# Performance work log

Measured on AMD Instinct MI355X. Metric: run time of the kernel, lower is better.

## Reference

```python
import jax, jax.numpy as jnp
import numpy as np

B, C, H, W = 4, 64, 256, 256
P, PRIOR, HID, HEADS, NPROMPT = 4, 64, 128, 4, 4
TOKEN = C * P * P  # 1024
RATIO = 0.25


def _patchify(x):
    b, c, h, w = x.shape
    gh, gw = h // P, w // P
    t = x.reshape(b, c, gh, P, gw, P).transpose(0, 2, 4, 1, 3, 5).reshape(b, gh * gw, c * P * P)
    return t, (b, c, gh, gw)


def _unpatchify(t, meta):
    b, c, gh, gw = meta
    return t.reshape(b, gh, gw, c, P, P).transpose(0, 3, 1, 4, 2, 5).reshape(b, c, gh * P, gw * P)


def _coords(gh, gw):
    ys = (jnp.arange(gh, dtype=jnp.float32) + 0.5) / gh
    xs = (jnp.arange(gw, dtype=jnp.float32) + 0.5) / gw
    yy, xx = jnp.meshgrid(ys, xs, indexing='ij')
    return jnp.stack([yy.ravel(), xx.ravel()], axis=-1)  # [N, 2]


def setup_inputs():
    key = jax.random.key(0)
    ks = iter(jax.random.split(key, 32))
    rn = lambda *s: jax.random.normal(next(ks), s, jnp.float32)
    w = lambda *s: rn(*s) * 0.02
    z = lambda *s: jnp.zeros(s, jnp.float32)
    return dict(
        vis_feat=rn(B, C, H, W),
        ir_feat=rn(B, C, H, W),
        prompt_bank=w(NPROMPT, PRIOR),
        Wr=w(2 * C, NPROMPT), br=z(NPROMPT),
        br_Wtok=w(2, 2 * TOKEN, HID), br_Wpri=w(2, PRIOR, HID), br_Wco=w(2, 2, HID),
        br_bs=z(2, HID), br_Wout=w(2, HID), br_bout=z(2),
        br_Wq=w(2, TOKEN, HID), br_Wk=w(2, TOKEN, HID), br_Wv=w(2, TOKEN, HID),
        br_Wo=w(2, HID, TOKEN), br_Wint=w(2, PRIOR, HID),
        br_Wbyp=w(2, 2 * TOKEN, TOKEN), br_bbyp=z(2, TOKEN),
        conv1_w=w(C, C, 3, 3), conv1_b=z(C),
        conv2_w=w(C, C, 3, 3), conv2_b=z(C),
        Wa1=w(PRIOR, 2 * C), ba1=z(2 * C),
        Wa2=w(2 * C, 2 * C), ba2=z(2 * C),
    )


def reference(vis_feat, ir_feat, prompt_bank, Wr, br, br_Wtok, br_Wpri, br_Wco, br_bs, br_Wout, br_bout, br_Wq, br_Wk, br_Wv, br_Wo, br_Wint, br_Wbyp, br_bbyp, conv1_w, conv1_b, conv2_w, conv2_b, Wa1, ba1, Wa2, ba2):
    # intent router: pooled features -> prompt mixture -> intent vector
    pooled = jnp.concatenate([vis_feat.mean((2, 3)), ir_feat.mean((2, 3))], -1)  # [B, 2C]
    prompt_weight = jax.nn.softmax(pooled @ Wr + br, -1)  # [B, NPROMPT]
    intent = prompt_weight @ prompt_bank  # [B, PRIOR]

    def split(x):
        F = jnp.fft.fft2(x)
        return jnp.abs(F), jnp.angle(F)

    vamp, vph = split(vis_feat)
    iamp, iph = split(ir_feat)

    def fuse(vm, im, i):
        vt, meta = _patchify(vm)
        it_, _ = _patchify(im)
        b, c, gh, gw = meta
        n = gh * gw
        coords = _coords(gh, gw)
        # token score net: tokens + intent + coord embedding -> scalar score per token
        h = (jnp.concatenate([vt, it_], -1) @ br_Wtok[i]
             + (intent @ br_Wpri[i])[:, None, :]
             + (coords @ br_Wco[i])[None] + br_bs[i])
        score = jax.nn.gelu(h) @ br_Wout[i] + br_bout[i]  # [B, N]
        k = max(1, int(n * RATIO))
        topk_val, topk_idx = jax.lax.top_k(score, k)
        gth = lambda t: jnp.take_along_axis(t, topk_idx[:, :, None], axis=1)
        vs, irs = gth(vt), gth(it_)  # [B, k, TOKEN]
        # selected-token cross attention (vis queries, ir keys/values), intent-modulated
        dh = HID // HEADS
        hd = lambda x, Wm: (x @ Wm).reshape(b, k, HEADS, dh)
        q, kk, vv = hd(vs, br_Wq[i]), hd(irs, br_Wk[i]), hd(irs, br_Wv[i])
        attn = jax.nn.softmax(jnp.einsum('bqhd,bkhd->bhqk', q, kk) / jnp.float32(np.sqrt(dh)), -1)
        o = jnp.einsum('bhqk,bkhd->bqhd', attn, vv).reshape(b, k, HID)
        o = o + (intent @ br_Wint[i])[:, None, :]
        fused_sel = vs + o @ br_Wo[i]  # [B, k, TOKEN]
        # lightweight bypass on all tokens (gated blend), then scatter selected back
        g = jax.nn.sigmoid(jnp.concatenate([vt, it_], -1) @ br_Wbyp[i] + br_bbyp[i])
        full = g * vt + (1.0 - g) * it_
        full = full.at[jnp.arange(b)[:, None], topk_idx].set(fused_sel)
        return _unpatchify(full, meta)

    famp = fuse(vamp, iamp, 0)
    fph = fuse(vph, iph, 1)
    fph = jnp.arctan2(jnp.sin(fph), jnp.cos(fph))  # phase wrap to (-pi, pi]
    spec = jax.lax.complex(famp * jnp.cos(fph), famp * jnp.sin(fph))
    spatial = jnp.fft.ifft2(spec).real

    conv = lambda x, wgt, bia: jax.lax.conv_general_dilated(
        x, wgt, (1, 1), 'SAME', dimension_numbers=('NCHW', 'OIHW', 'NCHW')) + bia[None, :, None, None]
    y = conv(jax.nn.relu(conv(spatial, conv1_w, conv1_b)), conv2_w, conv2_b)
    aff = jax.nn.gelu(intent @ Wa1 + ba1) @ Wa2 + ba2  # [B, 2C]
    gamma, beta = aff[:, :C], aff[:, C:]
    y = y * (1.0 + 0.1 * jnp.tanh(gamma))[:, :, None, None] + 0.1 * beta[:, :, None, None]
    return y + 0.5 * (vis_feat + ir_feat)
```

## Files before the change

kernel.cpp:

```cpp
#include <hip/hip_runtime.h>

typedef unsigned int uint;
typedef unsigned long long u64;
typedef __attribute__((ext_vector_type(8))) short short8;
typedef __attribute__((ext_vector_type(4))) float f32x4;

__device__ __forceinline__ uint brev8(uint x){ return __brev(x) >> 24; }
__device__ __forceinline__ float geluf(float x){
  return 0.5f*x*(1.f + tanhf(0.7978845608028654f*(x + 0.044715f*x*x*x)));
}
__device__ __forceinline__ unsigned short f2bf(float f){
  unsigned u = __float_as_uint(f);
  unsigned r = u + 0x7FFFu + ((u >> 16) & 1u);
  return (unsigned short)(r >> 16);
}
__device__ __forceinline__ float bf2f(unsigned short u){
  return __uint_as_float((uint)u << 16);
}

__global__ __launch_bounds__(256) void kern_pool(const float* __restrict__ vis,
                                                 const float* __restrict__ irf,
                                                 float* __restrict__ pooled){
  __shared__ float red[256];
  int bc = blockIdx.x;
  int b = bc >> 7, cc = bc & 127;
  const float* src = (cc < 64) ? (vis + (size_t)(b*64+cc)*65536)
                               : (irf + (size_t)(b*64+(cc-64))*65536);
  float s = 0.f;
  for (int i = threadIdx.x; i < 65536; i += 256) s += src[i];
  red[threadIdx.x] = s;
  __syncthreads();
  for (int off = 128; off > 0; off >>= 1){
    if (threadIdx.x < off) red[threadIdx.x] += red[threadIdx.x + off];
    __syncthreads();
  }
  if (threadIdx.x == 0) pooled[bc] = red[0] * (1.f/65536.f);
}

__global__ __launch_bounds__(256) void kern_small(const float* __restrict__ pooled,
    const float* __restrict__ Wr, const float* __restrict__ br,
    const float* __restrict__ bank, const float* __restrict__ Wpri,
    const float* __restrict__ Wint, const float* __restrict__ Wa1,
    const float* __restrict__ ba1, const float* __restrict__ Wa2,
    const float* __restrict__ ba2,
    float* __restrict__ IP, float* __restrict__ IPint,
    float* __restrict__ modg, float* __restrict__ modb){
  __shared__ float logit_s[16];
  __shared__ float pw_s[16];
  __shared__ float intent_s[4][64];
  __shared__ float t1_s[4][128];
  int t = threadIdx.x;
  if (t < 16){
    int b = t >> 2, j = t & 3;
    float s = br[j];
    for (int k = 0; k < 128; ++k) s += pooled[b*128+k]*Wr[k*4+j];
    logit_s[t] = s;
  }
  __syncthreads();
  if (t < 4){
    int b = t;
    float m = logit_s[b*4];
    for (int j = 1; j < 4; ++j) m = fmaxf(m, logit_s[b*4+j]);
    float e[4], sum = 0.f;
    for (int j = 0; j < 4; ++j){ e[j] = expf(logit_s[b*4+j]-m); sum += e[j]; }
    for (int j = 0; j < 4; ++j) pw_s[b*4+j] = e[j]/sum;
  }
  __syncthreads();
  {
    int b = t >> 6, p = t & 63;
    float s = 0.f;
    for (int j = 0; j < 4; ++j) s += pw_s[b*4+j]*bank[j*64+p];
    intent_s[b][p] = s;
  }
  __syncthreads();
  for (int o = t; o < 1024; o += 256){
    int i = o >> 9, rem = o & 511, b = rem >> 7, n = rem & 127;
    float s1 = 0.f, s2 = 0.f;
    for (int p = 0; p < 64; ++p){
      float iv = intent_s[b][p];
      s1 += iv * Wpri[(i*64+p)*128 + n];
      s2 += iv * Wint[(i*64+p)*128 + n];
    }
    IP[o] = s1; IPint[o] = s2;
  }
  for (int o = t; o < 512; o += 256){
    int b = o >> 7, n = o & 127;
    float s = ba1[n];
    for (int p = 0; p < 64; ++p) s += intent_s[b][p]*Wa1[p*128+n];
    t1_s[b][n] = geluf(s);
  }
  __syncthreads();
  for (int o = t; o < 512; o += 256){
    int b = o >> 7, n = o & 127;
    float s = ba2[n];
    for (int p = 0; p < 128; ++p) s += t1_s[b][p]*Wa2[p*128+n];
    if (n < 64) modg[b*64+n] = 1.f + 0.1f*tanhf(s);
    else        modb[b*64+(n-64)] = 0.1f*s;
  }
}

__global__ __launch_bounds__(256) void kern_fft_rows_fwd(const float* __restrict__ x,
    float* __restrict__ sre, float* __restrict__ sim){
  __shared__ float re[2][256], im[2][256];
  __shared__ float twr[128], twi[128];
  int t = threadIdx.x;
  if (t < 128){
    float a = -6.2831853071795864f * (float)t * (1.f/256.f);
    sincosf(a, &twi[t], &twr[t]);
  }
  int r = t >> 7, jj = t & 127;
  size_t row = (size_t)blockIdx.x*2 + r;
  {
    const float* xp = x + row*256;
    re[r][jj] = xp[jj]; re[r][jj+128] = xp[jj+128];
    im[r][jj] = 0.f;    im[r][jj+128] = 0.f;
  }
  __syncthreads();
  for (int s = 0; s < 8; ++s){
    int half = 128 >> s;
    int j = jj & (half-1);
    int g = jj >> (7-s);
    int k = (g << (8-s)) + j;
    int m = j << s;
    float wc = twr[m], ws = twi[m];
    float are = re[r][k],      aim = im[r][k];
    float bre = re[r][k+half], bim = im[r][k+half];
    re[r][k] = are + bre; im[r][k] = aim + bim;
    float tr = are - bre, ti = aim - bim;
    re[r][k+half] = tr*wc - ti*ws;
    im[r][k+half] = tr*ws + ti*wc;
    __syncthreads();
  }
  {
    float* orp = sre + row*256; float* oip = sim + row*256;
    int w1 = jj, w2 = jj + 128;
    orp[w1] = re[r][brev8(w1)]; oip[w1] = im[r][brev8(w1)];
    orp[w2] = re[r][brev8(w2)]; oip[w2] = im[r][brev8(w2)];
  }
}

__global__ __launch_bounds__(256) void kern_ifft_rows_spec(const float* __restrict__ famp,
    const float* __restrict__ fph, float* __restrict__ sre, float* __restrict__ sim){
  __shared__ float re[4][256], im[4][256];
  __shared__ float twr[128], twi[128];
  int t = threadIdx.x;
  if (t < 128){
    float a = -6.2831853071795864f * (float)t * (1.f/256.f);
    sincosf(a, &twi[t], &twr[t]);
  }
  int R = blockIdx.x * 4;
  {
    int r = t >> 6, q = t & 63;
    int row = R + r;
    int bc = row >> 8, h = row & 255;
    int b = bc >> 6, c = bc & 63;
    size_t addr = ((size_t)(b*4096 + (h>>2)*64 + q))*1024 + c*16 + (h&3)*4;
    float4 a4 = *(const float4*)(famp + addr);
    float4 p4 = *(const float4*)(fph + addr);
    float sn, cs;
    sincosf(p4.x, &sn, &cs); re[r][4*q+0] = a4.x*cs; im[r][4*q+0] = a4.x*sn;
    sincosf(p4.y, &sn, &cs); re[r][4*q+1] = a4.y*cs; im[r][4*q+1] = a4.y*sn;
    sincosf(p4.z, &sn, &cs); re[r][4*q+2] = a4.z*cs; im[r][4*q+2] = a4.z*sn;
    sincosf(p4.w, &sn, &cs); re[r][4*q+3] = a4.w*cs; im[r][4*q+3] = a4.w*sn;
  }
  __syncthreads();
  for (int s = 0; s < 8; ++s){
    int half = 128 >> s;
    #pragma unroll
    for (int bi0 = 0; bi0 < 2; ++bi0){
      int bi = t + bi0*256;
      int r = bi >> 7, tj = bi & 127;
      int j = tj & (half-1);
      int g = tj >> (7-s);
      int k = (g << (8-s)) + j;
      int m = j << s;
      float wc = twr[m], ws = -twi[m];
      float are = re[r][k],      aim = im[r][k];
      float bre = re[r][k+half], bim = im[r][k+half];
      re[r][k] = are + bre; im[r][k] = aim + bim;
      float tr = are - bre, ti = aim - bim;
      re[r][k+half] = tr*wc - ti*ws;
      im[r][k+half] = tr*ws + ti*wc;
    }
    __syncthreads();
  }
  {
    int r = t >> 6, q = t & 63;
    size_t row = (size_t)R + r;
    float4 vr, vi;
    vr.x = re[r][brev8(4*q+0)]; vi.x = im[r][brev8(4*q+0)];
    vr.y = re[r][brev8(4*q+1)]; vi.y = im[r][brev8(4*q+1)];
    vr.z = re[r][brev8(4*q+2)]; vi.z = im[r][brev8(4*q+2)];
    vr.w = re[r][brev8(4*q+3)]; vi.w = im[r][brev8(4*q+3)];
    *(float4*)(sre + row*256 + 4*q) = vr;
    *(float4*)(sim + row*256 + 4*q) = vi;
  }
}

template<int DIR>
__global__ __launch_bounds__(256) void kern_fft_cols(const float* __restrict__ sre,
    const float* __restrict__ sim, void* __restrict__ out0, void* __restrict__ out1){
  __shared__ float reL[256*17];
  __shared__ float imL[256*17];
  __shared__ float twr[128], twi[128];
  int t = threadIdx.x;
  if (t < 128){
    float a = -6.2831853071795864f * (float)t * (1.f/256.f);
    sincosf(a, &twi[t], &twr[t]);
  }
  int img = blockIdx.x >> 4;
  int c0 = (blockIdx.x & 15) * 16;
  {
    const float* pr = sre + ((size_t)img*256 + t)*256 + c0;
    const float* pi = sim + ((size_t)img*256 + t)*256 + c0;
    #pragma unroll
    for (int p = 0; p < 4; ++p){
      float4 vr = *(const float4*)(pr + 4*p);
      float4 vi = *(const float4*)(pi + 4*p);
      int base = t*17 + 4*p;
      reL[base+0]=vr.x; reL[base+1]=vr.y; reL[base+2]=vr.z; reL[base+3]=vr.w;
      imL[base+0]=vi.x; imL[base+1]=vi.y; imL[base+2]=vi.z; imL[base+3]=vi.w;
    }
  }
  __syncthreads();
  int col = t & 15, tb = t >> 4;
  for (int s = 0; s < 8; ++s){
    int half = 128 >> s;
    #pragma unroll
    for (int it = 0; it < 8; ++it){
      int tj = tb + it*16;
      int j = tj & (half-1);
      int g = tj >> (7-s);
      int k = (g << (8-s)) + j;
      int m = j << s;
      float wc = twr[m];
      float ws = (DIR == 0) ? twi[m] : -twi[m];
      int i0 = k*17 + col, i1 = (k+half)*17 + col;
      float are = reL[i0], aim = imL[i0];
      float bre = reL[i1], bim = imL[i1];
      reL[i0] = are + bre; imL[i0] = aim + bim;
      float tr = are - bre, ti = aim - bim;
      reL[i1] = tr*wc - ti*ws;
      imL[i1] = tr*ws + ti*wc;
    }
    __syncthreads();
  }
  int b = img >> 6, c = img & 63;
  int h = t; int src = (int)brev8((uint)h);
  if (DIR == 0){
    unsigned short* oa = (unsigned short*)out0;
    unsigned short* op = (unsigned short*)out1;
    int gy = h >> 2, py = h & 3;
    #pragma unroll
    for (int p = 0; p < 4; ++p){
      int base = src*17 + 4*p;
      float a0, a1, a2, a3, p0, p1, p2, p3;
      float rr, ii;
      rr = reL[base+0]; ii = imL[base+0]; a0 = sqrtf(rr*rr+ii*ii); p0 = atan2f(ii, rr);
      rr = reL[base+1]; ii = imL[base+1]; a1 = sqrtf(rr*rr+ii*ii); p1 = atan2f(ii, rr);
      rr = reL[base+2]; ii = imL[base+2]; a2 = sqrtf(rr*rr+ii*ii); p2 = atan2f(ii, rr);
      rr = reL[base+3]; ii = imL[base+3]; a3 = sqrtf(rr*rr+ii*ii); p3 = atan2f(ii, rr);
      size_t addr = ((size_t)(b*4096 + gy*64 + (c0>>2) + p))*1024 + c*16 + py*4;
      uint2 av, pv;
      av.x = (uint)f2bf(a0) | ((uint)f2bf(a1) << 16);
      av.y = (uint)f2bf(a2) | ((uint)f2bf(a3) << 16);
      pv.x = (uint)f2bf(p0) | ((uint)f2bf(p1) << 16);
      pv.y = (uint)f2bf(p2) | ((uint)f2bf(p3) << 16);
      *(uint2*)(oa + addr) = av;
      *(uint2*)(op + addr) = pv;
    }
  } else {
    float* op = (float*)out0 + ((size_t)img*256 + h)*256 + c0;
    #pragma unroll
    for (int p = 0; p < 4; ++p){
      int base = src*17 + 4*p;
      float4 v;
      v.x = reL[base+0]*(1.f/65536.f);
      v.y = reL[base+1]*(1.f/65536.f);
      v.z = reL[base+2]*(1.f/65536.f);
      v.w = reL[base+3]*(1.f/65536.f);
      *(float4*)(op + 4*p) = v;
    }
  }
}

struct TRS {
  const float* src[10];
  unsigned short* dst[10];
  int K[10], N[10];
  int start[11];
};
__global__ __launch_bounds__(256) void kern_tr(TRS p){
  __shared__ float lds[32][33];
  int bid = blockIdx.x;
  int e = 0;
  while (bid >= p.start[e+1]) ++e;
  int tloc = bid - p.start[e];
  int tilesN = p.N[e] >> 5;
  int tn = tloc % tilesN, tk = tloc / tilesN;
  int k0 = tk << 5, n0 = tn << 5;
  const float* src = p.src[e];
  unsigned short* dst = p.dst[e];
  int K = p.K[e], N = p.N[e];
  int r = threadIdx.x >> 5, c = threadIdx.x & 31;
  #pragma unroll
  for (int i = 0; i < 4; ++i)
    lds[r + 8*i][c] = src[(size_t)(k0 + r + 8*i)*N + n0 + c];
  __syncthreads();
  #pragma unroll
  for (int i = 0; i < 4; ++i)
    dst[(size_t)(n0 + r + 8*i)*K + k0 + c] = f2bf(lds[c][r + 8*i]);
}

struct GP2 {
  const unsigned short* A0[6];
  const unsigned short* A1[2];
  const unsigned short* Bt[6];
  float* Cm[6];
  const int* idxp[6];
  const float* ep0[2];
  const float* ep1[2];
  const float* ep2[2];
  int N, K;
};

template<int AMODE, int EPI>
__global__ __launch_bounds__(256) void kern_mgemm2(GP2 p){
  __shared__ __align__(16) unsigned short Asb[64*64];
  __shared__ __align__(16) unsigned short Bsb[128*64];
  __shared__ int idx_s[64];
  int z = blockIdx.z;
  const unsigned short* A0 = p.A0[z];
  const unsigned short* Bt = p.Bt[z];
  float* Cm = p.Cm[z];
  int tid = threadIdx.x;
  int m0 = blockIdx.x * 64;
  int n0 = blockIdx.y * 128;
  int lane = tid & 63, w = tid >> 6;
  int wr = w & 1, wc = w >> 1;
  int lr = lane & 15, ql = lane >> 4;

  if (AMODE == 2){
    if (tid < 64){
      int m = m0 + tid;
      idx_s[tid] = p.idxp[z][(m >> 10)*1024 + (m & 1023)];
    }
    __syncthreads();
  }
  int gb = m0 >> 10;

  f32x4 acc[2][4];
  #pragma unroll
  for (int i = 0; i < 2; ++i)
    #pragma unroll
    for (int j = 0; j < 4; ++j) acc[i][j] = (f32x4){0.f,0.f,0.f,0.f};

  int kh = tid & 7;
  int rA = tid >> 3;
  for (int k0 = 0; k0 < p.K; k0 += 64){
    #pragma unroll
    for (int s = 0; s < 2; ++s){
      int m = rA + 32*s;
      const unsigned short* ap;
      if (AMODE == 1){
        const unsigned short* srcp = (k0 < 1024) ? A0 : p.A1[z];
        ap = srcp + (size_t)(m0+m)*1024 + (k0 & 1023) + kh*8;
      } else {
        ap = A0 + ((size_t)(gb << 12) + idx_s[m])*(size_t)p.K + k0 + kh*8;
      }
      short8 v = *(const short8*)ap;
      int byte = m*128 + ((kh*16) ^ ((m & 7)*16));
      *(short8*)((char*)Asb + byte) = v;
    }
    #pragma unroll
    for (int s = 0; s < 4; ++s){
      int n = rA + 32*s;
      short8 v = *(const short8*)(Bt + (size_t)(n0+n)*p.K + k0 + kh*8);
      int byte = n*128 + ((kh*16) ^ ((n & 7)*16));
      *(short8*)((char*)Bsb + byte) = v;
    }
    __syncthreads();
    short8 af[2][2], bf[4][2];
    #pragma unroll
    for (int fm = 0; fm < 2; ++fm){
      int row = wr*32 + fm*16 + lr;
      #pragma unroll
      for (int kq = 0; kq < 2; ++kq){
        int byte = row*128 + ((kq*64 + ql*16) ^ ((row & 7)*16));
        af[fm][kq] = *(const short8*)((const char*)Asb + byte);
      }
    }
    #pragma unroll
    for (int fn = 0; fn < 4; ++fn){
      int row = wc*64 + fn*16 + lr;
      #pragma unroll
      for (int kq = 0; kq < 2; ++kq){
        int byte = row*128 + ((kq*64 + ql*16) ^ ((row & 7)*16));
        bf[fn][kq] = *(const short8*)((const char*)Bsb + byte);
      }
    }
    #pragma unroll
    for (int kq = 0; kq < 2; ++kq)
      #pragma unroll
      for (int fm = 0; fm < 2; ++fm)
        #pragma unroll
        for (int fn = 0; fn < 4; ++fn)
          acc[fm][fn] = __builtin_amdgcn_mfma_f32_16x16x32_bf16(af[fm][kq], bf[fn][kq],
                                                                acc[fm][fn], 0, 0, 0);
    __syncthreads();
  }

  #pragma unroll
  for (int fm = 0; fm < 2; ++fm){
    #pragma unroll
    for (int fn = 0; fn < 4; ++fn){
      int n = n0 + wc*64 + fn*16 + lr;
      #pragma unroll
      for (int reg = 0; reg < 4; ++reg){
        int m = m0 + wr*32 + fm*16 + ql*4 + reg;
        float v = acc[fm][fn][reg];
        if (EPI == 0){
          Cm[(size_t)m*p.N + n] = v;
        } else {
          int bl = m >> 12, g = m & 4095;
          int gy = g >> 6, gx = g & 63;
          float cy = ((float)gy + 0.5f)*(1.f/64.f);
          float cx = ((float)gx + 0.5f)*(1.f/64.f);
          float o = v + p.ep0[z][bl*128 + n] + cy*p.ep1[z][n]
                  + cx*p.ep1[z][128 + n] + p.ep2[z][n];
          Cm[(size_t)m*128 + n] = o;
        }
      }
    }
  }
}

struct GP3 {
  const unsigned short* A0[2];
  const unsigned short* A1[2];
  const unsigned short* Bt[2];
  float* Cm[2];
  const float* bias[2];
  const unsigned short* vt[2];
  const unsigned short* it[2];
  int K;
};

__global__ __launch_bounds__(256) void kern_mgemm3(GP3 p){
  __shared__ __align__(16) unsigned short Asb[128*64];
  __shared__ __align__(16) unsigned short Bsb[128*64];
  int z = blockIdx.z;
  const unsigned short* Bt = p.Bt[z];
  float* Cm = p.Cm[z];
  int tid = threadIdx.x;
  int m0 = blockIdx.x * 128;
  int n0 = blockIdx.y * 128;
  int lane = tid & 63, w = tid >> 6;
  int wr = w & 1, wc = w >> 1;
  int lr = lane & 15, ql = lane >> 4;

  f32x4 acc[4][4];
  #pragma unroll
  for (int i = 0; i < 4; ++i)
    #pragma unroll
    for (int j = 0; j < 4; ++j) acc[i][j] = (f32x4){0.f,0.f,0.f,0.f};

  int kh = tid & 7;
  int rA = tid >> 3;
  for (int k0 = 0; k0 < p.K; k0 += 64){
    const unsigned short* Asrc = (k0 < 1024) ? p.A0[z] : p.A1[z];
    int kk = (k0 & 1023) + kh*8;
    #pragma unroll
    for (int s = 0; s < 4; ++s){
      int m = rA + 32*s;
      short8 v = *(const short8*)(Asrc + (size_t)(m0+m)*1024 + kk);
      int byte = m*128 + ((kh*16) ^ ((m & 7)*16));
      *(short8*)((char*)Asb + byte) = v;
    }
    #pragma unroll
    for (int s = 0; s < 4; ++s){
      int n = rA + 32*s;
      short8 v = *(const short8*)(Bt + (size_t)(n0+n)*p.K + k0 + kh*8);
      int byte = n*128 + ((kh*16) ^ ((n & 7)*16));
      *(short8*)((char*)Bsb + byte) = v;
    }
    __syncthreads();
    short8 af[4][2], bf[4][2];
    #pragma unroll
    for (int fm = 0; fm < 4; ++fm){
      int row = wr*64 + fm*16 + lr;
      #pragma unroll
      for (int kq = 0; kq < 2; ++kq){
        int byte = row*128 + ((kq*64 + ql*16) ^ ((row & 7)*16));
        af[fm][kq] = *(const short8*)((const char*)Asb + byte);
      }
    }
    #pragma unroll
    for (int fn = 0; fn < 4; ++fn){
      int row = wc*64 + fn*16 + lr;
      #pragma unroll
      for (int kq = 0; kq < 2; ++kq){
        int byte = row*128 + ((kq*64 + ql*16) ^ ((row & 7)*16));
        bf[fn][kq] = *(const short8*)((const char*)Bsb + byte);
      }
    }
    #pragma unroll
    for (int kq = 0; kq < 2; ++kq)
      #pragma unroll
      for (int fm = 0; fm < 4; ++fm)
        #pragma unroll
        for (int fn = 0; fn < 4; ++fn)
          acc[fm][fn] = __builtin_amdgcn_mfma_f32_16x16x32_bf16(af[fm][kq], bf[fn][kq],
                                                                acc[fm][fn], 0, 0, 0);
    __syncthreads();
  }

  const unsigned short* vtp = p.vt[z];
  const unsigned short* itp = p.it[z];
  #pragma unroll
  for (int fm = 0; fm < 4; ++fm){
    #pragma unroll
    for (int fn = 0; fn < 4; ++fn){
      int n = n0 + wc*64 + fn*16 + lr;
      float bia = p.bias[z][n];
      #pragma unroll
      for (int reg = 0; reg < 4; ++reg){
        int m = m0 + wr*64 + fm*16 + ql*4 + reg;
        size_t off = (size_t)m*1024 + n;
        float vt = bf2f(vtp[off]);
        float it = bf2f(itp[off]);
        float gg = 1.f/(1.f + expf(-(acc[fm][fn][reg] + bia)));
        Cm[off] = gg*vt + (1.f-gg)*it;
      }
    }
  }
}

struct SCP {
  const float* A0[2];
  const float* Bm[2];
  float* Cm[2];
  const int* idxp[2];
  const unsigned short* vtb[2];
};

__global__ __launch_bounds__(256) void kern_scat(SCP p){
  __shared__ __align__(16) unsigned short Asb[64*40];
  __shared__ __align__(16) unsigned short Bsb[128*40];
  __shared__ int idx_s[64];
  int z = blockIdx.z;
  const float* A0 = p.A0[z];
  const float* Bm = p.Bm[z];
  float* Cm = p.Cm[z];
  int tid = threadIdx.x;
  int m0 = blockIdx.y * 64;
  int n0 = blockIdx.x * 128;
  int lane = tid & 63, w = tid >> 6;
  int wr = w & 1, wc = w >> 1;
  int lr = lane & 15, ql = lane >> 4;
  if (tid < 64){
    int m = m0 + tid;
    idx_s[tid] = p.idxp[z][(m >> 10)*1024 + (m & 1023)];
  }
  __syncthreads();
  int gb = m0 >> 10;

  f32x4 acc[2][4];
  #pragma unroll
  for (int i = 0; i < 2; ++i)
    #pragma unroll
    for (int j = 0; j < 4; ++j) acc[i][j] = (f32x4){0.f,0.f,0.f,0.f};

  for (int k0 = 0; k0 < 128; k0 += 32){
    {
      int m = tid & 63;
      int khh = (tid >> 6) * 8;
      const float* ap = A0 + (size_t)(m0+m)*128 + k0 + khh;
      float4 f0 = *(const float4*)ap;
      float4 f1 = *(const float4*)(ap + 4);
      short8 v;
      v[0]=(short)f2bf(f0.x); v[1]=(short)f2bf(f0.y);
      v[2]=(short)f2bf(f0.z); v[3]=(short)f2bf(f0.w);
      v[4]=(short)f2bf(f1.x); v[5]=(short)f2bf(f1.y);
      v[6]=(short)f2bf(f1.z); v[7]=(short)f2bf(f1.w);
      *(short8*)&Asb[m*40 + khh] = v;
    }
    #pragma unroll
    for (int e0 = 0; e0 < 512; e0 += 256){
      int e = e0 + tid;
      int n = e & 127;
      int khh = (e >> 7) * 8;
      const float* bp = Bm + (size_t)(k0+khh)*1024 + n0 + n;
      short8 v;
      #pragma unroll
      for (int j = 0; j < 8; ++j) v[j] = (short)f2bf(bp[(size_t)j*1024]);
      *(short8*)&Bsb[n*40 + khh] = v;
    }
    __syncthreads();
    short8 af[2], bf[4];
    #pragma unroll
    for (int fr = 0; fr < 2; ++fr)
      af[fr] = *(const short8*)&Asb[(wr*32 + fr*16 + lr)*40 + ql*8];
    #pragma unroll
    for (int fc = 0; fc < 4; ++fc)
      bf[fc] = *(const short8*)&Bsb[(wc*64 + fc*16 + lr)*40 + ql*8];
    #pragma unroll
    for (int fr = 0; fr < 2; ++fr)
      #pragma unroll
      for (int fc = 0; fc < 4; ++fc)
        acc[fr][fc] = __builtin_amdgcn_mfma_f32_16x16x32_bf16(af[fr], bf[fc],
                                                              acc[fr][fc], 0, 0, 0);
    __syncthreads();
  }

  #pragma unroll
  for (int fr = 0; fr < 2; ++fr){
    #pragma unroll
    for (int fc = 0; fc < 4; ++fc){
      int n = n0 + wc*64 + fc*16 + lr;
      #pragma unroll
      for (int reg = 0; reg < 4; ++reg){
        int mloc = wr*32 + fr*16 + ql*4 + reg;
        int gt = idx_s[mloc];
        size_t off = ((size_t)(gb << 12) + gt)*1024 + n;
        Cm[off] = acc[fr][fc][reg] + bf2f(p.vtb[z][off]);
      }
    }
  }
}

__global__ __launch_bounds__(64) void kern_score(const float* __restrict__ h,
    const float* __restrict__ wout, const float* __restrict__ bout,
    float* __restrict__ score, int Mper){
  int m = blockIdx.x, br = blockIdx.y, t = threadIdx.x;
  const float* hp = h + ((size_t)br*Mper + m)*128;
  const float* wp = wout + br*128;
  float s = geluf(hp[t])*wp[t] + geluf(hp[t+64])*wp[t+64];
  #pragma unroll
  for (int off = 32; off > 0; off >>= 1) s += __shfl_down(s, off);
  if (t == 0) score[(size_t)br*Mper + m] = s + bout[br];
}

__global__ __launch_bounds__(1024) void kern_topk(const float* __restrict__ score,
    int* __restrict__ idx_out){
  __shared__ u64 keys[4096];
  int b = blockIdx.x, t = threadIdx.x;
  for (int i = t; i < 4096; i += 1024){
    float s = score[b*4096 + i];
    uint u = __float_as_uint(s);
    uint msk = (u & 0x80000000u) ? ~u : (u | 0x80000000u);
    keys[i] = ((u64)msk << 32) | (uint)(4095 - i);
  }
  __syncthreads();
  for (int k = 2; k <= 4096; k <<= 1){
    for (int j = k >> 1; j > 0; j >>= 1){
      for (int i = t; i < 4096; i += 1024){
        int l = i ^ j;
        if (l > i){
          u64 a = keys[i], c = keys[l];
          bool descB = ((i & k) == 0);
          bool sw = descB ? (a < c) : (a > c);
          if (sw){ keys[i] = c; keys[l] = a; }
        }
      }
      __syncthreads();
    }
  }
  idx_out[b*1024 + t] = 4095 - (int)(keys[t] & 0xFFFFFFFFu);
}

__global__ __launch_bounds__(128) void kern_attn_part(const float* __restrict__ qb,
    const float* __restrict__ kb, const float* __restrict__ vb,
    float* __restrict__ paoa, float* __restrict__ pml){
  __shared__ float Ks[64][32];
  __shared__ float Vs[64][32];
  int t = threadIdx.x;
  int hh = blockIdx.y;
  int zc = blockIdx.z;
  int zf = zc >> 2, c = zc & 3;
  size_t boff = (size_t)zf*131072;
  int jq = blockIdx.x*128 + t;
  float qv[32];
  {
    const float4* qp = (const float4*)(qb + boff + (size_t)jq*128 + hh*32);
    #pragma unroll
    for (int d = 0; d < 8; ++d) ((float4*)qv)[d] = qp[d];
  }
  float mrun = -3.0e38f, lrun = 0.f;
  float oa[32];
  #pragma unroll
  for (int d = 0; d < 32; ++d) oa[d] = 0.f;
  for (int kt = 0; kt < 4; ++kt){
    int k0 = c*256 + kt*64;
    #pragma unroll
    for (int rep = 0; rep < 4; ++rep){
      int f = t + rep*128;
      int r = f >> 3, q4 = f & 7;
      size_t base = boff + (size_t)(k0 + r)*128 + hh*32 + 4*q4;
      *(float4*)&Ks[r][4*q4] = *(const float4*)(kb + base);
      *(float4*)&Vs[r][4*q4] = *(const float4*)(vb + base);
    }
    __syncthreads();
    #pragma unroll
    for (int st = 0; st < 4; ++st){
      float s[16];
      #pragma unroll
      for (int j = 0; j < 16; ++j){
        float v = 0.f;
        #pragma unroll
        for (int d = 0; d < 32; ++d) v += qv[d]*Ks[st*16+j][d];
        s[j] = v * 0.17677669529663687f;
      }
      float mt = s[0];
      #pragma unroll
      for (int j = 1; j < 16; ++j) mt = fmaxf(mt, s[j]);
      float mnew = fmaxf(mrun, mt);
      float alpha = expf(mrun - mnew);
      lrun *= alpha;
      #pragma unroll
      for (int d = 0; d < 32; ++d) oa[d] *= alpha;
      #pragma unroll
      for (int j = 0; j < 16; ++j){
        float pe = expf(s[j] - mnew);
        lrun += pe;
        #pragma unroll
        for (int d = 0; d < 32; ++d) oa[d] += pe*Vs[st*16+j][d];
      }
      mrun = mnew;
    }
    __syncthreads();
  }
  size_t rec = (((size_t)zf*4 + hh)*4 + c)*1024 + jq;
  float* pp = paoa + rec*32;
  #pragma unroll
  for (int d = 0; d < 8; ++d) ((float4*)pp)[d] = ((float4*)oa)[d];
  pml[rec*2]   = mrun;
  pml[rec*2+1] = lrun;
}

__global__ __launch_bounds__(256) void kern_attn_comb(const float* __restrict__ paoa,
    const float* __restrict__ pml, float* __restrict__ ob,
    const float* __restrict__ ipint, int PB, int b0){
  int t = threadIdx.x;
  int hh = blockIdx.y, zf = blockIdx.z;
  int jq = blockIdx.x*256 + t;
  size_t rbase = (((size_t)zf*4 + hh)*4)*1024 + jq;
  float mc[4], lc[4];
  #pragma unroll
  for (int c = 0; c < 4; ++c){
    mc[c] = pml[(rbase + c*1024)*2];
    lc[c] = pml[(rbase + c*1024)*2 + 1];
  }
  float M = fmaxf(fmaxf(mc[0], mc[1]), fmaxf(mc[2], mc[3]));
  float wgt[4], L = 0.f;
  #pragma unroll
  for (int c = 0; c < 4; ++c){ wgt[c] = expf(mc[c] - M); L += lc[c]*wgt[c]; }
  float inv = 1.f/L;
  int br = (zf >= PB) ? 1 : 0;
  int bb = zf - br*PB;
  const float* ip = ipint + br*512 + (b0+bb)*128 + hh*32;
  float* op = ob + (size_t)zf*131072 + (size_t)jq*128 + hh*32;
  #pragma unroll
  for (int d = 0; d < 32; ++d){
    float o = 0.f;
    #pragma unroll
    for (int c = 0; c < 4; ++c) o += paoa[(rbase + c*1024)*32 + d]*wgt[c];
    op[d] = o*inv + ip[d];
  }
}

__global__ __launch_bounds__(256) void kern_wt(const float* __restrict__ w1,
    const float* __restrict__ w2, unsigned short* __restrict__ wt){
  int blk = blockIdx.x;
  const float* src = (blk < 9) ? w1 : w2;
  int tap = blk - (blk < 9 ? 0 : 9);
  unsigned short* dst = wt + (blk < 9 ? 0 : 36864) + tap*4096;
  for (int e = threadIdx.x; e < 4096; e += 256){
    dst[e] = f2bf(src[(size_t)e*9 + tap]);
  }
}

template<int MODE>
__global__ __launch_bounds__(256) void kern_cmfma(const float* __restrict__ in,
    const unsigned short* __restrict__ wt, const float* __restrict__ bias,
    float* __restrict__ out,
    const float* __restrict__ modg, const float* __restrict__ modb,
    const float* __restrict__ vis, const float* __restrict__ irf){
  __shared__ __align__(16) unsigned short ins[64][268];
  int t = threadIdx.x;
  int y = blockIdx.x, b = blockIdx.y;
  int lane = t & 63, w = t >> 6;
  int wc = w & 1, wx = w >> 1;
  int lr = lane & 15, ql = lane >> 4;

  f32x4 acc[2][8];
  #pragma unroll
  for (int f = 0; f < 2; ++f)
    #pragma unroll
    for (int xf = 0; xf < 8; ++xf) acc[f][xf] = (f32x4){0.f,0.f,0.f,0.f};

  for (int dy = 0; dy < 3; ++dy){
    int yy = y + dy - 1;
    if (yy < 0 || yy > 255) continue;
    const float* src = in + ((size_t)(b*64)*256 + yy)*256;
    #pragma unroll
    for (int s = 0; s < 16; ++s){
      int e = t + s*256;
      int ci = e >> 6, q = e & 63;
      float4 f4 = *(const float4*)(src + (size_t)ci*65536 + 4*q);
      uint lo = (uint)f2bf(f4.x) | ((uint)f2bf(f4.y) << 16);
      uint hi = (uint)f2bf(f4.z) | ((uint)f2bf(f4.w) << 16);
      *(uint2*)&ins[ci][4*q + 4] = make_uint2(lo, hi);
    }
    if (t < 128){
      int r = t & 63;
      ins[r][(t >> 6) ? 260 : 3] = 0;
    }
    __syncthreads();
    short8 wf[2][3][2];
    #pragma unroll
    for (int kk = 0; kk < 2; ++kk)
      #pragma unroll
      for (int dx = 0; dx < 3; ++dx)
        #pragma unroll
        for (int f = 0; f < 2; ++f)
          wf[kk][dx][f] = *(const short8*)(wt +
            (size_t)((dy*3 + dx)*64 + 32*wc + 16*f + lr)*64 + kk*32 + ql*8);
    #pragma unroll
    for (int kk = 0; kk < 2; ++kk){
      const unsigned short* bp = &ins[kk*32 + ql*8][0];
      #pragma unroll
      for (int dx = 0; dx < 3; ++dx){
        int xb = 128*wx + lr + dx + 3;
        #pragma unroll
        for (int xf = 0; xf < 8; ++xf){
          int xi = xb + 16*xf;
          short8 bf;
          #pragma unroll
          for (int e = 0; e < 8; ++e) bf[e] = (short)bp[e*268 + xi];
          acc[0][xf] = __builtin_amdgcn_mfma_f32_16x16x32_bf16(wf[kk][dx][0], bf,
                                                               acc[0][xf], 0, 0, 0);
          acc[1][xf] = __builtin_amdgcn_mfma_f32_16x16x32_bf16(wf[kk][dx][1], bf,
                                                               acc[1][xf], 0, 0, 0);
        }
      }
    }
    __syncthreads();
  }

  #pragma unroll
  for (int f = 0; f < 2; ++f){
    #pragma unroll
    for (int xf = 0; xf < 8; ++xf){
      int x = 128*wx + 16*xf + lr;
      #pragma unroll
      for (int reg = 0; reg < 4; ++reg){
        int co = 32*wc + 16*f + ql*4 + reg;
        float v = acc[f][xf][reg] + bias[co];
        size_t oi = ((size_t)(b*64 + co)*256 + y)*256 + x;
        if (MODE == 1){
          out[oi] = fmaxf(v, 0.f);
        } else {
          out[oi] = v*modg[b*64+co] + modb[b*64+co] + 0.5f*(vis[oi] + irf[oi]);
        }
      }
    }
  }
}

extern "C" void kernel_launch(void* const* d_in, const int* in_sizes, int n_in,
                              void* d_out, int out_size, void* d_ws, size_t ws_size,
                              hipStream_t stream){
  (void)in_sizes; (void)n_in; (void)out_size;
  const float* vis  = (const float*)d_in[0];
  const float* irf  = (const float*)d_in[1];
  const float* bank = (const float*)d_in[2];
  const float* Wr   = (const float*)d_in[3];
  const float* br   = (const float*)d_in[4];
  const float* Wtok = (const float*)d_in[5];
  const float* Wpri = (const float*)d_in[6];
  const float* Wco  = (const float*)d_in[7];
  const float* bs   = (const float*)d_in[8];
  const float* Wout = (const float*)d_in[9];
  const float* bout = (const float*)d_in[10];
  const float* Wq   = (const float*)d_in[11];
  const float* Wk   = (const float*)d_in[12];
  const float* Wv   = (const float*)d_in[13];
  const float* Wo   = (const float*)d_in[14];
  const float* Wint = (const float*)d_in[15];
  const float* Wbyp = (const float*)d_in[16];
  const float* bbyp = (const float*)d_in[17];
  const float* c1w  = (const float*)d_in[18];
  const float* c1b  = (const float*)d_in[19];
  const float* c2w  = (const float*)d_in[20];
  const float* c2b  = (const float*)d_in[21];
  const float* Wa1  = (const float*)d_in[22];
  const float* ba1  = (const float*)d_in[23];
  const float* Wa2  = (const float*)d_in[24];
  const float* ba2  = (const float*)d_in[25];

  auto needB = [](int PB)->size_t{
    return ((size_t)PB*14755840 + 2792448) * 4;
  };
  const int PB = (ws_size >= needB(4)) ? 4 : (ws_size >= needB(2)) ? 2 : 1;

  float* ws = (float*)d_ws;
  const size_t PLF = (size_t)PB*4194304;
  float* PH4 = ws;
  unsigned short* ABV = (unsigned short*)(ws + PLF);
  unsigned short* PBV = ABV + PLF;
  unsigned short* ABI = PBV + PLF;
  unsigned short* PBI = ABI + PLF;
  float* S0 = ws + PLF;
  float* S1 = S0 + PLF;
  float* sm = ws + 3*PLF;
  float* hbuf  = sm; sm += (size_t)2*PB*524288;
  float* qbuf  = sm; sm += (size_t)2*PB*131072;
  float* kbuf  = sm; sm += (size_t)2*PB*131072;
  float* vbuf  = sm; sm += (size_t)2*PB*131072;
  float* obuf  = sm; sm += (size_t)2*PB*131072;
  float* score = sm; sm += (size_t)2*PB*4096;
  int*   idxb  = (int*)sm; sm += (size_t)2*PB*1024;
  float* pml   = sm; sm += (size_t)PB*65536;
  unsigned short* BTtok = (unsigned short*)sm;
  unsigned short* BTbyp = BTtok + 524288;
  unsigned short* BTq   = BTbyp + 4194304;
  unsigned short* BTk   = BTq + 262144;
  unsigned short* BTv   = BTk + 262144;
  sm += 2752512;
  float* pooled= sm; sm += 512;
  float* IP    = sm; sm += 1024;
  float* IPint = sm; sm += 1024;
  float* modg  = sm; sm += 256;
  float* modb  = sm; sm += 256;
  unsigned short* wtb = (unsigned short*)sm; sm += 36864;
  float* paoa = hbuf;

  kern_pool <<<512, 256, 0, stream>>>(vis, irf, pooled);
  kern_small<<<1, 256, 0, stream>>>(pooled, Wr, br, bank, Wpri, Wint,
                                    Wa1, ba1, Wa2, ba2, IP, IPint, modg, modb);
  kern_wt   <<<18, 256, 0, stream>>>(c1w, c2w, wtb);
  {
    TRS tr{};
    const float* srcs[10] = {Wtok, Wtok+262144, Wbyp, Wbyp+2097152,
                             Wq, Wq+131072, Wk, Wk+131072, Wv, Wv+131072};
    unsigned short* dsts[10] = {BTtok, BTtok+262144, BTbyp, BTbyp+2097152,
                                BTq, BTq+131072, BTk, BTk+131072, BTv, BTv+131072};
    int Ks[10] = {2048,2048,2048,2048,1024,1024,1024,1024,1024,1024};
    int Ns[10] = {128,128,1024,1024,128,128,128,128,128,128};
    int tiles[10] = {256,256,2048,2048,128,128,128,128,128,128};
    int acc0 = 0;
    for (int i = 0; i < 10; ++i){
      tr.src[i] = srcs[i]; tr.dst[i] = dsts[i];
      tr.K[i] = Ks[i]; tr.N[i] = Ns[i];
      tr.start[i] = acc0; acc0 += tiles[i];
    }
    tr.start[10] = acc0;
    kern_tr<<<acc0, 256, 0, stream>>>(tr);
  }

  for (int b0 = 0; b0 < 4; b0 += PB){
    const float* vis_b = vis + (size_t)b0*4194304;
    const float* ir_b  = irf + (size_t)b0*4194304;
    float* OUT = (float*)d_out + (size_t)b0*4194304;

    kern_fft_rows_fwd<<<PB*8192, 256, 0, stream>>>(vis_b, OUT, PH4);
    kern_fft_cols<0> <<<PB*1024, 256, 0, stream>>>(OUT, PH4, ABV, PBV);
    kern_fft_rows_fwd<<<PB*8192, 256, 0, stream>>>(ir_b, OUT, PH4);
    kern_fft_cols<0> <<<PB*1024, 256, 0, stream>>>(OUT, PH4, ABI, PBI);

    {
      GP2 p{};
      p.A0[0]=ABV; p.A1[0]=ABI; p.A0[1]=PBV; p.A1[1]=PBI;
      for (int z = 0; z < 2; ++z){
        p.Bt[z] = BTtok + (size_t)z*262144;
        p.Cm[z] = hbuf + (size_t)z*PB*524288;
        p.ep0[z] = IP + z*512 + b0*128;
        p.ep1[z] = Wco + z*256;
        p.ep2[z] = bs + z*128;
      }
      p.N = 128; p.K = 2048;
      kern_mgemm2<1,1><<<dim3(PB*64, 1, 2), 256, 0, stream>>>(p);
    }
    kern_score<<<dim3(PB*4096, 2), 64, 0, stream>>>(hbuf, Wout, bout, score, PB*4096);
    kern_topk <<<2*PB, 1024, 0, stream>>>(score, idxb);
    {
      GP3 p{};
      p.A0[0]=ABV; p.A1[0]=ABI; p.A0[1]=PBV; p.A1[1]=PBI;
      p.vt[0]=ABV; p.it[0]=ABI; p.vt[1]=PBV; p.it[1]=PBI;
      p.Cm[0]=OUT; p.Cm[1]=PH4;
      for (int z = 0; z < 2; ++z){
        p.Bt[z] = BTbyp + (size_t)z*2097152;
        p.bias[z] = bbyp + z*1024;
      }
      p.K = 2048;
      kern_mgemm3<<<dim3(PB*32, 8, 2), 256, 0, stream>>>(p);
    }
    {
      GP2 p{};
      const unsigned short* Aplanes[6] = {ABV, ABI, ABI, PBV, PBI, PBI};
      const unsigned short* Bmats[6] = {BTq, BTk, BTv,
                                        BTq+131072, BTk+131072, BTv+131072};
      float* Cms[6] = {qbuf, kbuf, vbuf,
                       qbuf+(size_t)PB*131072, kbuf+(size_t)PB*131072,
                       vbuf+(size_t)PB*131072};
      for (int z = 0; z < 6; ++z){
        p.A0[z] = Aplanes[z]; p.Bt[z] = Bmats[z]; p.Cm[z] = Cms[z];
        p.idxp[z] = idxb + (z < 3 ? 0 : PB*1024);
      }
      p.N = 128; p.K = 1024;
      kern_mgemm2<2,0><<<dim3(PB*16, 1, 6), 256, 0, stream>>>(p);
    }
    kern_attn_part<<<dim3(8, 4, 2*PB*4), 128, 0, stream>>>(qbuf, kbuf, vbuf,
                                                           paoa, pml);
    kern_attn_comb<<<dim3(4, 4, 2*PB), 256, 0, stream>>>(paoa, pml, obuf,
                                                         IPint, PB, b0);
    {
      SCP p{};
      p.A0[0]=obuf; p.A0[1]=obuf+(size_t)PB*131072;
      p.Bm[0]=Wo; p.Bm[1]=Wo+131072;
      p.Cm[0]=OUT; p.Cm[1]=PH4;
      p.vtb[0]=ABV; p.vtb[1]=PBV;
      p.idxp[0]=idxb; p.idxp[1]=idxb+PB*1024;
      kern_scat<<<dim3(8, PB*16, 2), 256, 0, stream>>>(p);
    }

    kern_ifft_rows_spec<<<PB*4096, 256, 0, stream>>>(OUT, PH4, S0, S1);
    kern_fft_cols<1>   <<<PB*1024, 256, 0, stream>>>(S0, S1, OUT, nullptr);
  }

  kern_cmfma<1><<<dim3(256, 4), 256, 0, stream>>>((float*)d_out, wtb, c1b, ws,
                                                  nullptr, nullptr, nullptr, nullptr);
  kern_cmfma<2><<<dim3(256, 4), 256, 0, stream>>>(ws, wtb + 36864, c2b, (float*)d_out,
                                                  modg, modb, vis, irf);
}
```

Baseline: 1.419 ms.

## Fuse token-score GEMM into bypass GEMM by concatenating weight matrices

The score-hidden GEMM (Wtok, N=128) and the bypass gate GEMM (Wbyp, N=1024) share the same A operand, the concatenated vis/ir amplitude or phase tokens. They are merged into one launch by storing both transposed weights contiguously (N=1152) and adding a ninth column-block whose epilogue writes the hidden activations with the coordinate and intent bias terms. This avoids a separate kernel launch and lets both GEMMs run in one grid. The merged kernel now runs before top-k, which is valid because the bypass output does not depend on top-k, though the extra epilogue branch may add some register pressure.

```diff
diff --git a/kernel.cpp b/kernel.cpp
--- a/kernel.cpp
+++ b/kernel.cpp
@@ -1,6 +1,7 @@
 #include <hip/hip_runtime.h>
 
 typedef unsigned int uint;
+typedef unsigned short ushort;
 typedef unsigned long long u64;
 typedef __attribute__((ext_vector_type(8))) short short8;
 typedef __attribute__((ext_vector_type(4))) float f32x4;
@@ -9,12 +10,12 @@
 __device__ __forceinline__ float geluf(float x){
   return 0.5f*x*(1.f + tanhf(0.7978845608028654f*(x + 0.044715f*x*x*x)));
 }
-__device__ __forceinline__ unsigned short f2bf(float f){
+__device__ __forceinline__ ushort f2bf(float f){
   unsigned u = __float_as_uint(f);
   unsigned r = u + 0x7FFFu + ((u >> 16) & 1u);
-  return (unsigned short)(r >> 16);
-}
-__device__ __forceinline__ float bf2f(unsigned short u){
+  return (ushort)(r >> 16);
+}
+__device__ __forceinline__ float bf2f(ushort u){
   return __uint_as_float((uint)u << 16);
 }
 
@@ -248,8 +249,8 @@
   int b = img >> 6, c = img & 63;
   int h = t; int src = (int)brev8((uint)h);
   if (DIR == 0){
-    unsigned short* oa = (unsigned short*)out0;
-    unsigned short* op = (unsigned short*)out1;
+    ushort* oa = (ushort*)out0;
+    ushort* op = (ushort*)out1;
     int gy = h >> 2, py = h & 3;
     #pragma unroll
     for (int p = 0; p < 4; ++p){
@@ -286,7 +287,7 @@
 
 struct TRS {
   const float* src[10];
-  unsigned short* dst[10];
+  ushort* dst[10];
   int K[10], N[10];
   int start[11];
 };
@@ -300,7 +301,7 @@
   int tn = tloc % tilesN, tk = tloc / tilesN;
   int k0 = tk << 5, n0 = tn << 5;
   const float* src = p.src[e];
-  unsigned short* dst = p.dst[e];
+  ushort* dst = p.dst[e];
   int K = p.K[e], N = p.N[e];
   int r = threadIdx.x >> 5, c = threadIdx.x & 31;
   #pragma unroll
@@ -313,25 +314,20 @@
 }
 
 struct GP2 {
-  const unsigned short* A0[6];
-  const unsigned short* A1[2];
-  const unsigned short* Bt[6];
+  const ushort* A0[6];
+  const ushort* Bt[6];
   float* Cm[6];
   const int* idxp[6];
-  const float* ep0[2];
-  const float* ep1[2];
-  const float* ep2[2];
   int N, K;
 };
 
-template<int AMODE, int EPI>
 __global__ __launch_bounds__(256) void kern_mgemm2(GP2 p){
-  __shared__ __align__(16) unsigned short Asb[64*64];
-  __shared__ __align__(16) unsigned short Bsb[128*64];
+  __shared__ __align__(16) ushort Asb[64*64];
+  __shared__ __align__(16) ushort Bsb[128*64];
   __shared__ int idx_s[64];
   int z = blockIdx.z;
-  const unsigned short* A0 = p.A0[z];
-  const unsigned short* Bt = p.Bt[z];
+  const ushort* A0 = p.A0[z];
+  const ushort* Bt = p.Bt[z];
   float* Cm = p.Cm[z];
   int tid = threadIdx.x;
   int m0 = blockIdx.x * 64;
@@ -340,13 +336,11 @@
   int wr = w & 1, wc = w >> 1;
   int lr = lane & 15, ql = lane >> 4;
 
-  if (AMODE == 2){
-    if (tid < 64){
-      int m = m0 + tid;
-      idx_s[tid] = p.idxp[z][(m >> 10)*1024 + (m & 1023)];
-    }
-    __syncthreads();
-  }
+  if (tid < 64){
+    int m = m0 + tid;
+    idx_s[tid] = p.idxp[z][(m >> 10)*1024 + (m & 1023)];
+  }
+  __syncthreads();
   int gb = m0 >> 10;
 
   f32x4 acc[2][4];
@@ -361,13 +355,7 @@
     #pragma unroll
     for (int s = 0; s < 2; ++s){
       int m = rA + 32*s;
-      const unsigned short* ap;
-      if (AMODE == 1){
-        const unsigned short* srcp = (k0 < 1024) ? A0 : p.A1[z];
-        ap = srcp + (size_t)(m0+m)*1024 + (k0 & 1023) + kh*8;
-      } else {
-        ap = A0 + ((size_t)(gb << 12) + idx_s[m])*(size_t)p.K + k0 + kh*8;
-      }
+      const ushort* ap = A0 + ((size_t)(gb << 12) + idx_s[m])*(size_t)p.K + k0 + kh*8;
       short8 v = *(const short8*)ap;
       int byte = m*128 + ((kh*16) ^ ((m & 7)*16));
       *(short8*)((char*)Asb + byte) = v;
@@ -418,40 +406,32 @@
       #pragma unroll
       for (int reg = 0; reg < 4; ++reg){
         int m = m0 + wr*32 + fm*16 + ql*4 + reg;
-        float v = acc[fm][fn][reg];
-        if (EPI == 0){
-          Cm[(size_t)m*p.N + n] = v;
-        } else {
-          int bl = m >> 12, g = m & 4095;
-          int gy = g >> 6, gx = g & 63;
-          float cy = ((float)gy + 0.5f)*(1.f/64.f);
-          float cx = ((float)gx + 0.5f)*(1.f/64.f);
-          float o = v + p.ep0[z][bl*128 + n] + cy*p.ep1[z][n]
-                  + cx*p.ep1[z][128 + n] + p.ep2[z][n];
-          Cm[(size_t)m*128 + n] = o;
-        }
+        Cm[(size_t)m*p.N + n] = acc[fm][fn][reg];
       }
     }
   }
 }
 
 struct GP3 {
-  const unsigned short* A0[2];
-  const unsigned short* A1[2];
-  const unsigned short* Bt[2];
+  const ushort* A0[2];
+  const ushort* A1[2];
+  const ushort* Bt[2];
+  float* Ch[2];
   float* Cm[2];
+  const float* ep0[2];
+  const float* ep1[2];
+  const float* ep2[2];
   const float* bias[2];
-  const unsigned short* vt[2];
-  const unsigned short* it[2];
+  const ushort* vt[2];
+  const ushort* it[2];
   int K;
 };
 
 __global__ __launch_bounds__(256) void kern_mgemm3(GP3 p){
-  __shared__ __align__(16) unsigned short Asb[128*64];
-  __shared__ __align__(16) unsigned short Bsb[128*64];
+  __shared__ __align__(16) ushort Asb[128*64];
+  __shared__ __align__(16) ushort Bsb[128*64];
   int z = blockIdx.z;
-  const unsigned short* Bt = p.Bt[z];
-  float* Cm = p.Cm[z];
+  const ushort* Bt = p.Bt[z];
   int tid = threadIdx.x;
   int m0 = blockIdx.x * 128;
   int n0 = blockIdx.y * 128;
@@ -468,7 +448,7 @@
   int kh = tid & 7;
   int rA = tid >> 3;
   for (int k0 = 0; k0 < p.K; k0 += 64){
-    const unsigned short* Asrc = (k0 < 1024) ? p.A0[z] : p.A1[z];
+    const ushort* Asrc = (k0 < 1024) ? p.A0[z] : p.A1[z];
     int kk = (k0 & 1023) + kh*8;
     #pragma unroll
     for (int s = 0; s < 4; ++s){
@@ -515,22 +495,46 @@
     __syncthreads();
   }
 
-  const unsigned short* vtp = p.vt[z];
-  const unsigned short* itp = p.it[z];
-  #pragma unroll
-  for (int fm = 0; fm < 4; ++fm){
-    #pragma unroll
-    for (int fn = 0; fn < 4; ++fn){
-      int n = n0 + wc*64 + fn*16 + lr;
-      float bia = p.bias[z][n];
-      #pragma unroll
-      for (int reg = 0; reg < 4; ++reg){
-        int m = m0 + wr*64 + fm*16 + ql*4 + reg;
-        size_t off = (size_t)m*1024 + n;
-        float vt = bf2f(vtp[off]);
-        float it = bf2f(itp[off]);
-        float gg = 1.f/(1.f + expf(-(acc[fm][fn][reg] + bia)));
-        Cm[off] = gg*vt + (1.f-gg)*it;
+  if (blockIdx.y == 0){
+    float* Ch = p.Ch[z];
+    #pragma unroll
+    for (int fm = 0; fm < 4; ++fm){
+      #pragma unroll
+      for (int fn = 0; fn < 4; ++fn){
+        int n = wc*64 + fn*16 + lr;
+        #pragma unroll
+        for (int reg = 0; reg < 4; ++reg){
+          int m = m0 + wr*64 + fm*16 + ql*4 + reg;
+          int bl = m >> 12, g = m & 4095;
+          int gy = g >> 6, gx = g & 63;
+          float cy = ((float)gy + 0.5f)*(1.f/64.f);
+          float cx = ((float)gx + 0.5f)*(1.f/64.f);
+          float o = acc[fm][fn][reg] + p.ep0[z][bl*128 + n] + cy*p.ep1[z][n]
+                  + cx*p.ep1[z][128 + n] + p.ep2[z][n];
+          Ch[(size_t)m*128 + n] = o;
+        }
+      }
+    }
+  } else {
+    float* Cm = p.Cm[z];
+    const ushort* vtp = p.vt[z];
+    const ushort* itp = p.it[z];
+    int nb = n0 - 128;
+    #pragma unroll
+    for (int fm = 0; fm < 4; ++fm){
+      #pragma unroll
+      for (int fn = 0; fn < 4; ++fn){
+        int n = nb + wc*64 + fn*16 + lr;
+        float bia = p.bias[z][n];
+        #pragma unroll
+        for (int reg = 0; reg < 4; ++reg){
+          int m = m0 + wr*64 + fm*16 + ql*4 + reg;
+          size_t off = (size_t)m*1024 + n;
+          float vt = bf2f(vtp[off]);
+          float it = bf2f(itp[off]);
+          float gg = 1.f/(1.f + expf(-(acc[fm][fn][reg] + bia)));
+          Cm[off] = gg*vt + (1.f-gg)*it;
+        }
       }
     }
   }
@@ -541,12 +545,12 @@
   const float* Bm[2];
   float* Cm[2];
   const int* idxp[2];
-  const unsigned short* vtb[2];
+  const ushort* vtb[2];
 };
 
 __global__ __launch_bounds__(256) void kern_scat(SCP p){
-  __shared__ __align__(16) unsigned short Asb[64*40];
-  __shared__ __align__(16) unsigned short Bsb[128*40];
+  __shared__ __align__(16) ushort Asb[64*40];
+  __shared__ __align__(16) ushort Bsb[128*40];
   __shared__ int idx_s[64];
   int z = blockIdx.z;
   const float* A0 = p.A0[z];
@@ -770,11 +774,11 @@
 }
 
 __global__ __launch_bounds__(256) void kern_wt(const float* __restrict__ w1,
-    const float* __restrict__ w2, unsigned short* __restrict__ wt){
+    const float* __restrict__ w2, ushort* __restrict__ wt){
   int blk = blockIdx.x;
   const float* src = (blk < 9) ? w1 : w2;
   int tap = blk - (blk < 9 ? 0 : 9);
-  unsigned short* dst = wt + (blk < 9 ? 0 : 36864) + tap*4096;
+  ushort* dst = wt + (blk < 9 ? 0 : 36864) + tap*4096;
   for (int e = threadIdx.x; e < 4096; e += 256){
     dst[e] = f2bf(src[(size_t)e*9 + tap]);
   }
@@ -782,11 +786,11 @@
 
 template<int MODE>
 __global__ __launch_bounds__(256) void kern_cmfma(const float* __restrict__ in,
-    const unsigned short* __restrict__ wt, const float* __restrict__ bias,
+    const ushort* __restrict__ wt, const float* __restrict__ bias,
     float* __restrict__ out,
     const float* __restrict__ modg, const float* __restrict__ modb,
     const float* __restrict__ vis, const float* __restrict__ irf){
-  __shared__ __align__(16) unsigned short ins[64][268];
+  __shared__ __align__(16) ushort ins[64][268];
   int t = threadIdx.x;
   int y = blockIdx.x, b = blockIdx.y;
   int lane = t & 63, w = t >> 6;
@@ -828,7 +832,7 @@
             (size_t)((dy*3 + dx)*64 + 32*wc + 16*f + lr)*64 + kk*32 + ql*8);
     #pragma unroll
     for (int kk = 0; kk < 2; ++kk){
-      const unsigned short* bp = &ins[kk*32 + ql*8][0];
+      const ushort* bp = &ins[kk*32 + ql*8][0];
       #pragma unroll
       for (int dx = 0; dx < 3; ++dx){
         int xb = 128*wx + lr + dx + 3;
@@ -907,10 +911,10 @@
   float* ws = (float*)d_ws;
   const size_t PLF = (size_t)PB*4194304;
   float* PH4 = ws;
-  unsigned short* ABV = (unsigned short*)(ws + PLF);
-  unsigned short* PBV = ABV + PLF;
-  unsigned short* ABI = PBV + PLF;
-  unsigned short* PBI = ABI + PLF;
+  ushort* ABV = (ushort*)(ws + PLF);
+  ushort* PBV = ABV + PLF;
+  ushort* ABI = PBV + PLF;
+  ushort* PBI = ABI + PLF;
   float* S0 = ws + PLF;
   float* S1 = S0 + PLF;
   float* sm = ws + 3*PLF;
@@ -922,18 +926,17 @@
   float* score = sm; sm += (size_t)2*PB*4096;
   int*   idxb  = (int*)sm; sm += (size_t)2*PB*1024;
   float* pml   = sm; sm += (size_t)PB*65536;
-  unsigned short* BTtok = (unsigned short*)sm;
-  unsigned short* BTbyp = BTtok + 524288;
-  unsigned short* BTq   = BTbyp + 4194304;
-  unsigned short* BTk   = BTq + 262144;
-  unsigned short* BTv   = BTk + 262144;
+  ushort* BTcomb = (ushort*)sm;
+  ushort* BTq    = BTcomb + 4718592;
+  ushort* BTk    = BTq + 262144;
+  ushort* BTv    = BTk + 262144;
   sm += 2752512;
   float* pooled= sm; sm += 512;
   float* IP    = sm; sm += 1024;
   float* IPint = sm; sm += 1024;
   float* modg  = sm; sm += 256;
   float* modb  = sm; sm += 256;
-  unsigned short* wtb = (unsigned short*)sm; sm += 36864;
+  ushort* wtb = (ushort*)sm; sm += 36864;
   float* paoa = hbuf;
 
   kern_pool <<<512, 256, 0, stream>>>(vis, irf, pooled);
@@ -944,8 +947,8 @@
     TRS tr{};
     const float* srcs[10] = {Wtok, Wtok+262144, Wbyp, Wbyp+2097152,
                              Wq, Wq+131072, Wk, Wk+131072, Wv, Wv+131072};
-    unsigned short* dsts[10] = {BTtok, BTtok+262144, BTbyp, BTbyp+2097152,
-                                BTq, BTq+131072, BTk, BTk+131072, BTv, BTv+131072};
+    ushort* dsts[10] = {BTcomb, BTcomb+2359296, BTcomb+262144, BTcomb+2359296+262144,
+                        BTq, BTq+131072, BTk, BTk+131072, BTv, BTv+131072};
     int Ks[10] = {2048,2048,2048,2048,1024,1024,1024,1024,1024,1024};
     int Ns[10] = {128,128,1024,1024,128,128,128,128,128,128};
     int tiles[10] = {256,256,2048,2048,128,128,128,128,128,128};
@@ -970,37 +973,27 @@
     kern_fft_cols<0> <<<PB*1024, 256, 0, stream>>>(OUT, PH4, ABI, PBI);
 
     {
-      GP2 p{};
-      p.A0[0]=ABV; p.A1[0]=ABI; p.A0[1]=PBV; p.A1[1]=PBI;
-      for (int z = 0; z < 2; ++z){
-        p.Bt[z] = BTtok + (size_t)z*262144;
-        p.Cm[z] = hbuf + (size_t)z*PB*524288;
-        p.ep0[z] = IP + z*512 + b0*128;
-        p.ep1[z] = Wco + z*256;
-        p.ep2[z] = bs + z*128;
-      }
-      p.N = 128; p.K = 2048;
-      kern_mgemm2<1,1><<<dim3(PB*64, 1, 2), 256, 0, stream>>>(p);
-    }
-    kern_score<<<dim3(PB*4096, 2), 64, 0, stream>>>(hbuf, Wout, bout, score, PB*4096);
-    kern_topk <<<2*PB, 1024, 0, stream>>>(score, idxb);
-    {
       GP3 p{};
       p.A0[0]=ABV; p.A1[0]=ABI; p.A0[1]=PBV; p.A1[1]=PBI;
       p.vt[0]=ABV; p.it[0]=ABI; p.vt[1]=PBV; p.it[1]=PBI;
       p.Cm[0]=OUT; p.Cm[1]=PH4;
       for (int z = 0; z < 2; ++z){
-        p.Bt[z] = BTbyp + (size_t)z*2097152;
+        p.Bt[z] = BTcomb + (size_t)z*2359296;
+        p.Ch[z] = hbuf + (size_t)z*PB*524288;
+        p.ep0[z] = IP + z*512 + b0*128;
+        p.ep1[z] = Wco + z*256;
+        p.ep2[z] = bs + z*128;
         p.bias[z] = bbyp + z*1024;
       }
       p.K = 2048;
-      kern_mgemm3<<<dim3(PB*32, 8, 2), 256, 0, stream>>>(p);
-    }
+      kern_mgemm3<<<dim3(PB*32, 9, 2), 256, 0, stream>>>(p);
+    }
+    kern_score<<<dim3(PB*4096, 2), 64, 0, stream>>>(hbuf, Wout, bout, score, PB*4096);
+    kern_topk <<<2*PB, 1024, 0, stream>>>(score, idxb);
     {
       GP2 p{};
-      const unsigned short* Aplanes[6] = {ABV, ABI, ABI, PBV, PBI, PBI};
-      const unsigned short* Bmats[6] = {BTq, BTk, BTv,
-                                        BTq+131072, BTk+131072, BTv+131072};
+      const ushort* Aplanes[6] = {ABV, ABI, ABI, PBV, PBI, PBI};
+      const ushort* Bmats[6] = {BTq, BTk, BTv, BTq+131072, BTk+131072, BTv+131072};
       float* Cms[6] = {qbuf, kbuf, vbuf,
                        qbuf+(size_t)PB*131072, kbuf+(size_t)PB*131072,
                        vbuf+(size_t)PB*131072};
@@ -1009,7 +1002,7 @@
         p.idxp[z] = idxb + (z < 3 ? 0 : PB*1024);
       }
       p.N = 128; p.K = 1024;
-      kern_mgemm2<2,0><<<dim3(PB*16, 1, 6), 256, 0, stream>>>(p);
+      kern_mgemm2<<<dim3(PB*16, 1, 6), 256, 0, stream>>>(p);
     }
     kern_attn_part<<<dim3(8, 4, 2*PB*4), 128, 0, stream>>>(qbuf, kbuf, vbuf,
                                                            paoa, pml);
```

After: 1.411 ms. Within noise of the previous version (-0.6%).
